# Kernel optimization log

Hardware: AMD Instinct MI355X
Metric: run time of the kernel (lower is better)

Reference implementation:

```python
import jax, jax.numpy as jnp
import numpy as np

SEQ_LEN = 4096
NUM_EIGH = 40
D_IN = 64
D_OUT = 64
K_U = 3
BSZ = 2


def _spectral_filters(L, K):
    # Hankel matrix Z_ij = 2/((i+j)^3 - (i+j)), i,j in [1, L]
    e = np.arange(1, L + 1, dtype=np.float64)
    s = e[:, None] + e[None, :]
    Z = 2.0 / (s ** 3 - s)
    sigma, phi = np.linalg.eigh(Z)
    phi_k = phi[:, -K:] * sigma[-K:] ** 0.25  # (L, K)
    return jnp.asarray(phi_k, dtype=jnp.float32)


def setup_inputs() -> dict:
    key = jax.random.key(0)
    kx, km, kp, kn = jax.random.split(key, 4)
    x = jax.random.normal(kx, (BSZ, SEQ_LEN, D_IN), dtype=jnp.float32)
    phi = _spectral_filters(SEQ_LEN, NUM_EIGH)  # (L, K)
    M = jax.random.normal(km, (D_OUT, D_IN, K_U), dtype=jnp.float32) / D_IN
    M_phi_plus = jax.random.normal(kp, (NUM_EIGH, D_IN, D_OUT), dtype=jnp.float32) / 10.0
    M_phi_minus = jax.random.normal(kn, (NUM_EIGH, D_IN, D_OUT), dtype=jnp.float32) / 10.0
    return {"x": x, "phi": phi, "M": M, "M_phi_plus": M_phi_plus, "M_phi_minus": M_phi_minus}


def _stu_forward(x, phi, M, M_phi_plus, M_phi_minus):
    bsz, L, d_in = x.shape
    n = int(2 ** np.ceil(np.log2(2 * L - 1)))  # FFT length (8192)
    t = jnp.arange(L)
    sgn = jnp.where(t % 2 == 1, -1.0, 1.0).astype(x.dtype)  # (L,)

    # FFT of [u, u*sgn] once over d_in (K-expansion deferred to freq domain; FFT is linear)
    U = jnp.stack([x, x * sgn[None, :, None]], axis=-1)        # (b, L, d, 2)
    U_f = jnp.fft.rfft(U, n=n, axis=1)                         # (b, nf, d, 2)
    v_f = jnp.fft.rfft(phi.astype(jnp.float32), n=n, axis=0)   # (nf, K)

    prod = v_f[None, :, :, None, None] * U_f[:, :, None, :, :]  # (b, nf, K, d, 2)
    U_conv = jnp.fft.irfft(prod, n=n, axis=1)[:, :L]            # (b, L, K, d, 2)
    U_plus = U_conv[..., 0]
    U_minus = U_conv[..., 1] * sgn[None, :, None, None]

    # spectral tensordot: contract (K, d_in) -> d_out
    spec = (jnp.einsum('blkd,kdo->blo', U_plus, M_phi_plus)
            + jnp.einsum('blkd,kdo->blo', U_minus, M_phi_minus))

    ar = jnp.zeros((bsz, L, M.shape[0]), dtype=x.dtype)
    for i in range(M.shape[2]):  # k_u is small and fixed
        y_i = jnp.einsum('bli,oi->blo', x, M[:, :, i])
        if i > 0:
            y_i = jnp.pad(y_i[:, : L - i], ((0, 0), (i, 0), (0, 0)))
        ar = ar + y_i
    return spec + ar


def reference(x, phi, M, M_phi_plus, M_phi_minus):
    return _stu_forward(x, phi, M, M_phi_plus, M_phi_minus)
```

## Files before the change

kernel.cpp:

```cpp
#include <hip/hip_runtime.h>

typedef short bf16x8 __attribute__((ext_vector_type(8)));
typedef float f32x4 __attribute__((ext_vector_type(4)));
typedef unsigned short u16;

__device__ __forceinline__ u16 f2bf(float f) {
    unsigned u = __builtin_bit_cast(unsigned, f);
    return (u16)((u + 0x7fffu + ((u >> 16) & 1u)) >> 16);
}

__global__ __launch_bounds__(256)
void k_pre(const float* __restrict__ Mp, const float* __restrict__ Mm,
           float* __restrict__ ApT, float* __restrict__ AmT,
           float* __restrict__ out, int* __restrict__ counter) {
    __shared__ float tp[64 * 65], tm[64 * 65];
    if (blockIdx.x < 40) {
        const int k = blockIdx.x, tid = threadIdx.x;
        for (int f = tid; f < 4096; f += 256) {
            int d = f >> 6, o = f & 63;
            float p = Mp[k * 4096 + f], m = Mm[k * 4096 + f];
            tp[o * 65 + d] = p + m;
            tm[o * 65 + d] = p - m;
        }
        __syncthreads();
        for (int f = tid; f < 4096; f += 256) {
            int o = f >> 6, d = f & 63;
            ApT[k * 4096 + f] = tp[o * 65 + d];
            AmT[k * 4096 + f] = tm[o * 65 + d];
        }
    } else {
        const int bz = blockIdx.x - 40;
        if (bz == 0 && threadIdx.x == 0) *counter = 0;
        float* po = out + bz * 4096;
        #pragma unroll
        for (int i = 0; i < 4; ++i)
            *(f32x4*)(po + (threadIdx.x + i * 256) * 4) = (f32x4){0.f, 0.f, 0.f, 0.f};
    }
}

__global__ __launch_bounds__(256)
void k_mid(const float* __restrict__ x, u16* __restrict__ xpad,
           const float* __restrict__ phi, const float* __restrict__ ApT,
           const float* __restrict__ AmT, const float* __restrict__ Mar,
           u16* __restrict__ wg) {
    if (blockIdx.x < 256) {
        const int u = blockIdx.x;
        #pragma unroll
        for (int i = 0; i < 4; ++i) {
            int gid = (u * 4 + i) * 256 + threadIdx.x;
            int b = gid >> 17, rem = gid & 131071;
            int r = rem >> 4, c4 = rem & 15;
            u16 o0 = 0, o1 = 0, o2 = 0, o3 = 0;
            if (r >= 4096) {
                const f32x4 v = *(const f32x4*)(x + ((b << 12) + (r - 4096)) * 64 + c4 * 4);
                o0 = f2bf(v.x); o1 = f2bf(v.y); o2 = f2bf(v.z); o3 = f2bf(v.w);
            }
            u16* p = xpad + ((b << 13) + r) * 64 + c4 * 4;
            p[0] = o0; p[1] = o1; p[2] = o2; p[3] = o3;
        }
    } else {
        const int bi  = blockIdx.x - 256;
        const int par = bi & 1;
        const int sbq = bi >> 1;
        const int sb  = sbq >> 4, qb = sbq & 15;
        const int q   = qb * 256 + threadIdx.x;
        const int o   = q >> 6, d = q & 63;
        const float* A = (par ? AmT : ApT);

        float a[40];
        #pragma unroll
        for (int k = 0; k < 40; ++k) a[k] = A[k * 4096 + q];

        #pragma unroll 2
        for (int m = 0; m < 32; ++m) {
            const int s = sb * 64 + 2 * m + par;
            const float* ph = phi + s * 40;
            float e0 = 0.f, e1 = 0.f;
            #pragma unroll
            for (int k = 0; k < 40; k += 2) { e0 += ph[k] * a[k]; e1 += ph[k + 1] * a[k + 1]; }
            float ev = e0 + e1;
            if (s < 3) ev += Mar[o * 192 + d * 3 + s];
            wg[(size_t)s * 4096 + q] = f2bf(ev);
        }
    }
}

__global__ __launch_bounds__(256, 2)
void k_spectral(const u16* __restrict__ xpad, const u16* __restrict__ wg,
                float* __restrict__ out, int* __restrict__ counter) {
    __shared__ __align__(16) u16 xs[2 * 191 * 64];
    __shared__ __align__(16) u16 wsm[2 * 64 * 64];
    __shared__ int sh;

    const int tid  = threadIdx.x;
    const int lane = tid & 63, w = tid >> 6;
    const int m15  = lane & 15, q4 = lane >> 4;
    const int par  = w >> 1, batch = w & 1;
    const int f0 = tid * 2, f1 = tid * 2 + 1;
    const int l0 = (((f0 >> 3) * 8) + ((f0 & 7) ^ ((f0 >> 3) & 7))) * 8;
    const int l1 = (((f1 >> 3) * 8) + ((f1 & 7) ^ ((f1 >> 3) & 7))) * 8;

    for (;;) {
        __syncthreads();
        if (tid == 0) sh = atomicAdd(counter, 1);
        __syncthreads();
        const int U = sh;
        if (U >= 1120) break;

        int mu = U, shalf = 0, slen = 64;
        if (U >= 992) { mu = 992 + ((U - 992) >> 1); shalf = (U - 992) & 1; slen = 32; }
        int g = 0;
        #pragma unroll 1
        while (g < 31 && (g + 1) * (64 - g) <= mu) ++g;
        const int rem = mu - g * (65 - g);
        const int cnt = 32 - g;
        const int col = (rem >= cnt) ? 1 : 0;
        const int J = 2 * g + col;
        const int I = g + (col ? rem - cnt : rem);
        const int t0 = I << 7, s0 = (J << 6) + (shalf << 5);
        const int nrows = 127 + slen;
        const int jmax = slen >> 1;
        const int base = 4096 + t0 - s0 - (slen - 1);

        const u16* wbase = wg + (size_t)s0 * 4096;
        bf16x8 pre[4];
        pre[0] = *(const bf16x8*)(wbase + f0 * 8);
        pre[1] = *(const bf16x8*)(wbase + f1 * 8);
        pre[2] = *(const bf16x8*)(wbase + 4096 + f0 * 8);
        pre[3] = *(const bf16x8*)(wbase + 4096 + f1 * 8);

        #pragma unroll
        for (int b = 0; b < 2; ++b) {
            #pragma unroll 1
            for (int f = tid; f < nrows * 8; f += 256) {
                int r = f >> 3, c = f & 7;
                bf16x8 v = *(const bf16x8*)(xpad + (size_t)((b << 13) + base + r) * 64 + c * 8);
                *(bf16x8*)(xs + ((b * 191 + r) * 8 + (c ^ (r & 7))) * 8) = v;
            }
        }

        f32x4 acc[8][4];
        #pragma unroll
        for (int mt = 0; mt < 8; ++mt)
            #pragma unroll
            for (int nt = 0; nt < 4; ++nt)
                acc[mt][nt] = (f32x4){0.f, 0.f, 0.f, 0.f};

        const u16* xb = xs + batch * (191 * 64);

        #pragma unroll 1
        for (int j = 0; j < jmax; ++j) {
            __syncthreads();
            *(bf16x8*)(wsm + l0)        = pre[0];
            *(bf16x8*)(wsm + l1)        = pre[1];
            *(bf16x8*)(wsm + 4096 + l0) = pre[2];
            *(bf16x8*)(wsm + 4096 + l1) = pre[3];
            __syncthreads();
            if (j < jmax - 1) {
                const u16* wp = wbase + (size_t)(2 * j + 2) * 4096;
                pre[0] = *(const bf16x8*)(wp + f0 * 8);
                pre[1] = *(const bf16x8*)(wp + f1 * 8);
                pre[2] = *(const bf16x8*)(wp + 4096 + f0 * 8);
                pre[3] = *(const bf16x8*)(wp + 4096 + f1 * 8);
            }
            const u16* wpar = wsm + par * 4096;
            const int ds = 2 * j + par;
            #pragma unroll
            for (int ks = 0; ks < 2; ++ks) {
                const int kq = ks * 4 + q4;
                bf16x8 bf[4];
                #pragma unroll
                for (int nt = 0; nt < 4; ++nt) {
                    int o = nt * 16 + m15;
                    bf[nt] = *(const bf16x8*)(wpar + (o * 8 + (kq ^ (o & 7))) * 8);
                }
                #pragma unroll
                for (int mt = 0; mt < 8; ++mt) {
                    int r = mt * 16 + m15 + (slen - 1) - ds;
                    bf16x8 av = *(const bf16x8*)(xb + (r * 8 + (kq ^ (r & 7))) * 8);
                    #pragma unroll
                    for (int nt = 0; nt < 4; ++nt)
                        acc[mt][nt] = __builtin_amdgcn_mfma_f32_16x16x32_bf16(
                            av, bf[nt], acc[mt][nt], 0, 0, 0);
                }
            }
        }

        float* fs = (float*)wsm;
        #pragma unroll
        for (int rd = 0; rd < 4; ++rd) {
            __syncthreads();
            if (par == 1) {
                #pragma unroll
                for (int i = 0; i < 8; ++i) {
                    int ti = rd * 8 + i;
                    *(f32x4*)(fs + (batch * 8 + i) * 256 + lane * 4) = acc[ti >> 2][ti & 3];
                }
            }
            __syncthreads();
            if (par == 0) {
                #pragma unroll
                for (int i = 0; i < 8; ++i) {
                    int ti = rd * 8 + i;
                    f32x4 v = *(const f32x4*)(fs + (batch * 8 + i) * 256 + lane * 4);
                    acc[ti >> 2][ti & 3] += v;
                }
            }
        }

        if (par == 0) {
            #pragma unroll
            for (int mt = 0; mt < 8; ++mt) {
                int t = t0 + mt * 16 + q4 * 4;
                #pragma unroll
                for (int nt = 0; nt < 4; ++nt) {
                    int o = nt * 16 + m15;
                    float* op = out + (size_t)((batch << 12) + t) * 64 + o;
                    #pragma unroll
                    for (int r = 0; r < 4; ++r)
                        atomicAdd(op + r * 64, acc[mt][nt][r]);
                }
            }
        }
    }
}

extern "C" void kernel_launch(void* const* d_in, const int* in_sizes, int n_in,
                              void* d_out, int out_size, void* d_ws, size_t ws_size,
                              hipStream_t stream) {
    const float* x   = (const float*)d_in[0];
    const float* phi = (const float*)d_in[1];
    const float* M   = (const float*)d_in[2];
    const float* Mp  = (const float*)d_in[3];
    const float* Mm  = (const float*)d_in[4];
    float* out = (float*)d_out;

    int* counter = (int*)d_ws;
    u16* xpad = (u16*)((char*)d_ws + 4096);
    u16* wg   = (u16*)((char*)d_ws + 4096 + 2097152);
    float* ApT = (float*)((char*)d_ws + 4096 + 2097152 + 33554432);
    float* AmT = ApT + 40 * 4096;

    k_pre<<<168, 256, 0, stream>>>(Mp, Mm, ApT, AmT, out, counter);
    k_mid<<<2304, 256, 0, stream>>>(x, xpad, phi, ApT, AmT, M, wg);
    k_spectral<<<512, 256, 0, stream>>>(xpad, wg, out, counter);
}
```

Measured before the change: 221.6 us.

## Load MFMA B-operand weights directly from global into registers, drop LDS staging

```diff
diff --git a/kernel.cpp b/kernel.cpp
--- a/kernel.cpp
+++ b/kernel.cpp
@@ -89,16 +89,12 @@
 void k_spectral(const u16* __restrict__ xpad, const u16* __restrict__ wg,
                 float* __restrict__ out, int* __restrict__ counter) {
     __shared__ __align__(16) u16 xs[2 * 191 * 64];
-    __shared__ __align__(16) u16 wsm[2 * 64 * 64];
     __shared__ int sh;
 
     const int tid  = threadIdx.x;
     const int lane = tid & 63, w = tid >> 6;
     const int m15  = lane & 15, q4 = lane >> 4;
     const int par  = w >> 1, batch = w & 1;
-    const int f0 = tid * 2, f1 = tid * 2 + 1;
-    const int l0 = (((f0 >> 3) * 8) + ((f0 & 7) ^ ((f0 >> 3) & 7))) * 8;
-    const int l1 = (((f1 >> 3) * 8) + ((f1 & 7) ^ ((f1 >> 3) & 7))) * 8;
 
     for (;;) {
         __syncthreads();
@@ -122,13 +118,6 @@
         const int jmax = slen >> 1;
         const int base = 4096 + t0 - s0 - (slen - 1);
 
-        const u16* wbase = wg + (size_t)s0 * 4096;
-        bf16x8 pre[4];
-        pre[0] = *(const bf16x8*)(wbase + f0 * 8);
-        pre[1] = *(const bf16x8*)(wbase + f1 * 8);
-        pre[2] = *(const bf16x8*)(wbase + 4096 + f0 * 8);
-        pre[3] = *(const bf16x8*)(wbase + 4096 + f1 * 8);
-
         #pragma unroll
         for (int b = 0; b < 2; ++b) {
             #pragma unroll 1
@@ -148,32 +137,12 @@
 
         const u16* xb = xs + batch * (191 * 64);
 
-        #pragma unroll 1
-        for (int j = 0; j < jmax; ++j) {
-            __syncthreads();
-            *(bf16x8*)(wsm + l0)        = pre[0];
-            *(bf16x8*)(wsm + l1)        = pre[1];
-            *(bf16x8*)(wsm + 4096 + l0) = pre[2];
-            *(bf16x8*)(wsm + 4096 + l1) = pre[3];
-            __syncthreads();
-            if (j < jmax - 1) {
-                const u16* wp = wbase + (size_t)(2 * j + 2) * 4096;
-                pre[0] = *(const bf16x8*)(wp + f0 * 8);
-                pre[1] = *(const bf16x8*)(wp + f1 * 8);
-                pre[2] = *(const bf16x8*)(wp + 4096 + f0 * 8);
-                pre[3] = *(const bf16x8*)(wp + 4096 + f1 * 8);
-            }
-            const u16* wpar = wsm + par * 4096;
-            const int ds = 2 * j + par;
+        const u16* wptr = wg + (size_t)(s0 + par) * 4096 + m15 * 64 + q4 * 8;
+
+        auto computeS = [&](int ds, bf16x8 (&bc)[4][2]) {
             #pragma unroll
             for (int ks = 0; ks < 2; ++ks) {
                 const int kq = ks * 4 + q4;
-                bf16x8 bf[4];
-                #pragma unroll
-                for (int nt = 0; nt < 4; ++nt) {
-                    int o = nt * 16 + m15;
-                    bf[nt] = *(const bf16x8*)(wpar + (o * 8 + (kq ^ (o & 7))) * 8);
-                }
                 #pragma unroll
                 for (int mt = 0; mt < 8; ++mt) {
                     int r = mt * 16 + m15 + (slen - 1) - ds;
@@ -181,12 +150,46 @@
                     #pragma unroll
                     for (int nt = 0; nt < 4; ++nt)
                         acc[mt][nt] = __builtin_amdgcn_mfma_f32_16x16x32_bf16(
-                            av, bf[nt], acc[mt][nt], 0, 0, 0);
-                }
-            }
-        }
-
-        float* fs = (float*)wsm;
+                            av, bc[nt][ks], acc[mt][nt], 0, 0, 0);
+                }
+            }
+        };
+
+        bf16x8 bA[4][2], bB[4][2];
+        #pragma unroll
+        for (int nt = 0; nt < 4; ++nt) {
+            bA[nt][0] = *(const bf16x8*)(wptr + nt * 1024);
+            bA[nt][1] = *(const bf16x8*)(wptr + nt * 1024 + 32);
+        }
+        __syncthreads();
+
+        #pragma unroll 1
+        for (int jj = 0; jj < (jmax >> 1); ++jj) {
+            const int ds0 = 4 * jj + par;
+            {
+                const u16* wn = wptr + 8192;
+                #pragma unroll
+                for (int nt = 0; nt < 4; ++nt) {
+                    bB[nt][0] = *(const bf16x8*)(wn + nt * 1024);
+                    bB[nt][1] = *(const bf16x8*)(wn + nt * 1024 + 32);
+                }
+                computeS(ds0, bA);
+            }
+            {
+                if (jj < (jmax >> 1) - 1) {
+                    const u16* wn = wptr + 16384;
+                    #pragma unroll
+                    for (int nt = 0; nt < 4; ++nt) {
+                        bA[nt][0] = *(const bf16x8*)(wn + nt * 1024);
+                        bA[nt][1] = *(const bf16x8*)(wn + nt * 1024 + 32);
+                    }
+                }
+                computeS(ds0 + 2, bB);
+            }
+            wptr += 16384;
+        }
+
+        float* fs = (float*)xs;
         #pragma unroll
         for (int rd = 0; rd < 4; ++rd) {
             __syncthreads();
```

Measured after the change: 281.8 us. 1.27x slower.
